# Kernel optimization log

Hardware: AMD Instinct MI355X
Metric: run time of the kernel (lower is better)

Reference implementation:

```python
import jax, jax.numpy as jnp
import numpy as np

SEQ, D, H = 4096, 1024, 1024


def setup_inputs() -> dict:
    key = jax.random.key(0)
    k_x, k_w1, k_b1, k_w2, k_b2 = jax.random.split(key, 5)
    std = 1.0 / np.sqrt(H)
    inputs = jax.random.normal(k_x, (SEQ, D), dtype=jnp.float32)
    W1 = jax.random.uniform(k_w1, (3 * H, 2 * D), minval=-std, maxval=std, dtype=jnp.float32)
    b1 = jax.random.uniform(k_b1, (3 * H,), minval=-std, maxval=std, dtype=jnp.float32)
    W2 = jax.random.uniform(k_w2, (H, H), minval=-std, maxval=std, dtype=jnp.float32)
    b2 = jax.random.uniform(k_b2, (H,), minval=-std, maxval=std, dtype=jnp.float32)
    return {"inputs": inputs, "W1": W1, "b1": b1, "W2": W2, "b2": b2}


def reference(inputs, W1, b1, W2, b2):
    # Exclusive prefix sum along seq: s[t] = sum_{i<t} x[i]
    s = jnp.concatenate(
        [jnp.zeros((1, inputs.shape[1]), dtype=inputs.dtype),
         jnp.cumsum(inputs[:-1], axis=0)], axis=0)
    v = jnp.concatenate([inputs, s], axis=1)            # [S, 2D]
    gates = v @ W1.T + b1                               # [S, 3H]
    ig, fg, h = jnp.split(gates, 3, axis=1)
    ig = jax.nn.sigmoid(ig)
    fg = jax.nn.sigmoid(fg)
    h = jnp.tanh(h) @ W2.T + b2                         # [S, H]
    hr = h * ig
    return (fg, hr)
```

## Files before the change

### kernel.cpp

```cpp
#include <hip/hip_runtime.h>
#include <cmath>

#define S_SEQ 4096
#define HD 1024
#define NG 3072
#define CHR 32
#define NCH 128

typedef _Float16 half8_t __attribute__((ext_vector_type(8)));
typedef _Float16 half4_t __attribute__((ext_vector_type(4)));
typedef float f32x4_t __attribute__((ext_vector_type(4)));

__device__ __forceinline__ void gload_lds16(const void* g, void* l) {
  __builtin_amdgcn_global_load_lds(
      (const __attribute__((address_space(1))) void*)g,
      (__attribute__((address_space(3))) void*)l, 16, 0, 0);
}

__device__ __forceinline__ float sigmoidf_(float x) {
  return 1.f / (1.f + __expf(-x));
}
__device__ __forceinline__ float tanhf_(float x) {
  return 1.f - 2.f / (__expf(2.f * x) + 1.f);
}

#define CONV_BLOCKS 7168
__global__ void prep(const float* __restrict__ W1, const float* __restrict__ W2,
                     _Float16* __restrict__ w1h, _Float16* __restrict__ w2h,
                     const float* __restrict__ x, _Float16* __restrict__ A,
                     _Float16* __restrict__ xsum) {
  const int bid = blockIdx.x;
  if (bid < CONV_BLOCKS) {
    const int n1 = NG * 2048 / 4;
    int i = bid * 256 + threadIdx.x;
    const float* src = (i < n1) ? (W1 + (size_t)i * 4)
                                : (W2 + (size_t)(i - n1) * 4);
    _Float16* dst = (i < n1) ? (w1h + (size_t)i * 4)
                             : (w2h + (size_t)(i - n1) * 4);
    float4 v = *(const float4*)src;
    half4_t h;
    h[0] = (_Float16)v.x; h[1] = (_Float16)v.y;
    h[2] = (_Float16)v.z; h[3] = (_Float16)v.w;
    *(half4_t*)dst = h;
  } else {
    const int sx = bid - CONV_BLOCKS;
    const int j = (sx & 3) * 256 + threadIdx.x;
    const int c = sx >> 2;
    const int t0 = c * CHR;
    float run = 0.f;
    for (int t = t0; t < t0 + CHR; ++t) {
      float v = x[(size_t)t * HD + j];
      A[(size_t)t * 2048 + j]        = (_Float16)v;
      A[(size_t)t * 2048 + 1024 + j] = (_Float16)run;
      run += v;
    }
    xsum[(size_t)c * HD + j] = (_Float16)run;
  }
}

__global__ void scan_part(const float* __restrict__ praw,
                          const float* __restrict__ b1,
                          float* __restrict__ pout) {
  int j = blockIdx.x * 256 + threadIdx.x;
  const size_t SP = (size_t)NCH * NG;
  float run = b1[j];
  for (int c = 0; c < NCH; c += 8) {
    float v[8];
#pragma unroll
    for (int u = 0; u < 8; ++u) {
      size_t i0 = (size_t)(c + u) * NG + j;
      v[u] = (praw[i0] + praw[i0 + SP]) + (praw[i0 + 2 * SP] + praw[i0 + 3 * SP]);
    }
#pragma unroll
    for (int u = 0; u < 8; ++u) {
      pout[(size_t)(c + u) * NG + j] = run;
      run += v[u];
    }
  }
}

__global__ __launch_bounds__(256, 2)
void gemm_part(const _Float16* __restrict__ A, const _Float16* __restrict__ B,
               float* __restrict__ C) {
  __shared__ _Float16 As[128 * 32];
  __shared__ _Float16 Bs[128 * 32];

  const int tid = threadIdx.x;
  const int lane = tid & 63;
  const int wid = tid >> 6;
  const int wr = wid >> 1;
  const int wc = wid & 1;

  const int n0 = blockIdx.x * 128;
  const int koff = blockIdx.z * 256;

  const int srow = lane >> 2;
  const int scol = (lane & 3) << 3;

  const _Float16* gA = A + (size_t)(wid * 32 + srow) * 1024 + koff + scol;
  const _Float16* gB = B + (size_t)(n0 + wid * 32 + srow) * 2048 + koff + scol;
  _Float16* lA = As + (wid * 32) * 32;
  _Float16* lB = Bs + (wid * 32) * 32;

  f32x4_t acc[4][4] = {};

  const int fr = lane & 15;
  const int fk = (lane >> 4) << 3;

  for (int kk = 0; kk < 256; kk += 32) {
    gload_lds16(gA + kk,                    lA);
    gload_lds16(gA + kk + (size_t)16*1024,  lA + 16 * 32);
    gload_lds16(gB + kk,                    lB);
    gload_lds16(gB + kk + (size_t)16*2048,  lB + 16 * 32);
    __syncthreads();

    half8_t af[4], bf[4];
#pragma unroll
    for (int m = 0; m < 4; ++m)
      af[m] = *(const half8_t*)&As[(wr * 64 + m * 16 + fr) * 32 + fk];
#pragma unroll
    for (int n = 0; n < 4; ++n)
      bf[n] = *(const half8_t*)&Bs[(wc * 64 + n * 16 + fr) * 32 + fk];
#pragma unroll
    for (int m = 0; m < 4; ++m)
#pragma unroll
      for (int n = 0; n < 4; ++n)
        acc[m][n] = __builtin_amdgcn_mfma_f32_16x16x32_f16(af[m], bf[n],
                                                           acc[m][n], 0, 0, 0);
    __syncthreads();
  }

  float* Cz = C + (size_t)blockIdx.z * NCH * NG;
  const int crow = wr * 64 + ((lane >> 4) << 2);
  const int ccol = n0 + wc * 64 + fr;
#pragma unroll
  for (int m = 0; m < 4; ++m)
#pragma unroll
    for (int n = 0; n < 4; ++n) {
      const int col = ccol + n * 16;
#pragma unroll
      for (int r = 0; r < 4; ++r)
        Cz[(size_t)(crow + m * 16 + r) * NG + col] = acc[m][n][r];
    }
}

#define BARX __builtin_amdgcn_s_barrier()
#define PR1 __builtin_amdgcn_s_setprio(1)
#define PR0 __builtin_amdgcn_s_setprio(0)
#define VM4 asm volatile("s_waitcnt vmcnt(4)" ::: "memory")

template <int NTILE, int MODE>
__global__ __launch_bounds__(256, 3)
void gemm_t3(const _Float16* __restrict__ A, const _Float16* __restrict__ B,
             int N,
             const float* __restrict__ part, _Float16* __restrict__ igb,
             float* __restrict__ outf, _Float16* __restrict__ th,
             const float* __restrict__ bias, const _Float16* __restrict__ mulh) {
  constexpr int KS = NTILE * 32;
  __shared__ __align__(16) _Float16 sA[3][128 * 32];
  __shared__ __align__(16) _Float16 sB[3][128 * 32];

  const int tid = threadIdx.x;
  const int l = tid & 63;
  const int wid = tid >> 6;
  const int wr = wid >> 1;
  const int wc = wid & 1;
  const int m0 = blockIdx.y * 128;
  const int n0 = blockIdx.x * 128;

  const int srow = tid >> 2;
  const int schunk = (tid & 3) ^ ((tid >> 3) & 3);
  const _Float16* gA = A + (size_t)(m0 + srow) * KS + schunk * 8;
  const _Float16* gB = B + (size_t)(n0 + srow) * KS + schunk * 8;
  const int ldst = tid * 8;

#define STG(bn, kt) do {                                              \
    const int kk_ = (kt) * 32;                                        \
    gload_lds16(gA + kk_,           &sA[bn][ldst]);                   \
    gload_lds16(gA + kk_ + 64 * KS, &sA[bn][2048 + ldst]);            \
    gload_lds16(gB + kk_,           &sB[bn][ldst]);                   \
    gload_lds16(gB + kk_ + 64 * KS, &sB[bn][2048 + ldst]);            \
  } while (0)

  const int fr = l & 15;
  const int kidx = (((l >> 4) ^ ((l >> 1) & 3)) << 3);

  f32x4_t acc[4][4] = {};

#define BODY(kt, bc, bn) do {                                         \
    int ks_ = (kt) + 2; if (ks_ > NTILE - 1) ks_ = NTILE - 1;         \
    STG(bn, ks_);                                                     \
    half8_t af[4], bf[4];                                             \
    _Pragma("unroll")                                                 \
    for (int m = 0; m < 4; ++m)                                       \
      af[m] = *(const half8_t*)&sA[bc][(wr*64 + m*16 + fr)*32 + kidx];\
    _Pragma("unroll")                                                 \
    for (int n = 0; n < 4; ++n)                                       \
      bf[n] = *(const half8_t*)&sB[bc][(wc*64 + n*16 + fr)*32 + kidx];\
    PR1;                                                              \
    _Pragma("unroll")                                                 \
    for (int m = 0; m < 4; ++m)                                       \
      _Pragma("unroll")                                               \
      for (int n = 0; n < 4; ++n)                                     \
        acc[m][n] = __builtin_amdgcn_mfma_f32_16x16x32_f16(           \
            af[m], bf[n], acc[m][n], 0, 0, 0);                        \
    PR0;                                                              \
    VM4; BARX;                                                        \
  } while (0)

  STG(0, 0);
  STG(1, 1);
  VM4; BARX;

#pragma unroll 1
  for (int t3 = 0; t3 < NTILE / 3; ++t3) {
    const int kt = t3 * 3;
    BODY(kt,     0, 2);
    BODY(kt + 1, 1, 0);
    BODY(kt + 2, 2, 1);
  }
  if constexpr (NTILE % 3 >= 1) BODY(NTILE - NTILE % 3,     0, 2);
  if constexpr (NTILE % 3 >= 2) BODY(NTILE - NTILE % 3 + 1, 1, 0);

  const int crow = m0 + wr * 64 + ((l >> 4) << 2);
  const int ccol = n0 + wc * 64 + fr;
#pragma unroll
  for (int m = 0; m < 4; ++m)
#pragma unroll
    for (int n = 0; n < 4; ++n) {
      const int col = ccol + n * 16;
#pragma unroll
      for (int r = 0; r < 4; ++r) {
        const int row = crow + m * 16 + r;
        const float v = acc[m][n][r];
        if (MODE == 1) {
          size_t idx = (size_t)row * N + col;
          outf[idx] = (v + bias[col]) * (float)mulh[idx];
        } else {
          float g = v + part[(size_t)(row >> 5) * NG + col];
          if (col < 1024)
            igb[(size_t)row * HD + col] = (_Float16)sigmoidf_(g);
          else if (col < 2048)
            outf[(size_t)row * HD + (col - 1024)] = sigmoidf_(g);
          else
            th[(size_t)row * HD + (col - 2048)] = (_Float16)tanhf_(g);
        }
      }
    }
#undef STG
#undef BODY
}

extern "C" void kernel_launch(void* const* d_in, const int* in_sizes, int n_in,
                              void* d_out, int out_size, void* d_ws, size_t ws_size,
                              hipStream_t stream) {
  const float* x  = (const float*)d_in[0];
  const float* W1 = (const float*)d_in[1];
  const float* b1 = (const float*)d_in[2];
  const float* W2 = (const float*)d_in[3];
  const float* b2 = (const float*)d_in[4];
  float* out0 = (float*)d_out;
  float* out1 = out0 + (size_t)S_SEQ * HD;

  char* ws = (char*)d_ws;
  _Float16* Ah    = (_Float16*)(ws);
  _Float16* w1h   = (_Float16*)(ws + ((size_t)16 << 20));
  _Float16* w2h   = (_Float16*)(ws + ((size_t)28 << 20));
  _Float16* xsumh = (_Float16*)(ws + ((size_t)30 << 20));
  float*    praw4 = (float*)   (ws + ((size_t)31 << 20));
  float*    pout  = (float*)   (ws + ((size_t)37 << 20));
  _Float16* igb   = (_Float16*)(ws + ((size_t)39 << 20));
  _Float16* th    = (_Float16*)(ws + ((size_t)47 << 20));

  prep<<<dim3(CONV_BLOCKS + 512), dim3(256), 0, stream>>>(
      W1, W2, w1h, w2h, x, Ah, xsumh);

  gemm_part<<<dim3(NG / 128, 1, 4), dim3(256), 0, stream>>>(
      xsumh, w1h + 1024, praw4);

  scan_part<<<dim3(NG / 256), dim3(256), 0, stream>>>(praw4, b1, pout);

  gemm_t3<64, 2><<<dim3(NG / 128, S_SEQ / 128), dim3(256), 0, stream>>>(
      Ah, w1h, NG, pout, igb, out0, th, nullptr, nullptr);

  gemm_t3<32, 1><<<dim3(HD / 128, S_SEQ / 128), dim3(256), 0, stream>>>(
      th, w2h, HD, nullptr, nullptr, out1, nullptr, b2, igb);
}
```

Baseline: 147.7 us.

## Replace first GEMM with 256x256-tile 8-wave phased kernel; vectorize prefix prep

The main gates GEMM moves from a 128x128 tile, triple-buffered kernel to a 512-thread kernel that computes a 256x256 tile with K=64 stages. It double-buffers in LDS, interleaves the global-to-LDS loads with four MFMA quarter-phases separated by barriers, and remaps block IDs so neighbouring blocks share tiles for cache reuse. The chunked prefix-sum prep is also vectorized to float4 per thread, using fewer blocks. The larger tile is meant to raise arithmetic intensity and cut redundant loads, at the cost of one wave of 192 blocks and heavier register and LDS use.

```diff
diff --git a/kernel.cpp b/kernel.cpp
--- a/kernel.cpp
+++ b/kernel.cpp
@@ -6,6 +6,7 @@
 #define NG 3072
 #define CHR 32
 #define NCH 128
+#define NT1 32
 
 typedef _Float16 half8_t __attribute__((ext_vector_type(8)));
 typedef _Float16 half4_t __attribute__((ext_vector_type(4)));
@@ -43,18 +44,25 @@
     h[2] = (_Float16)v.z; h[3] = (_Float16)v.w;
     *(half4_t*)dst = h;
   } else {
-    const int sx = bid - CONV_BLOCKS;
-    const int j = (sx & 3) * 256 + threadIdx.x;
-    const int c = sx >> 2;
+    const int c = bid - CONV_BLOCKS;
+    const int j = threadIdx.x * 4;
     const int t0 = c * CHR;
-    float run = 0.f;
+    float4 run = make_float4(0.f, 0.f, 0.f, 0.f);
     for (int t = t0; t < t0 + CHR; ++t) {
-      float v = x[(size_t)t * HD + j];
-      A[(size_t)t * 2048 + j]        = (_Float16)v;
-      A[(size_t)t * 2048 + 1024 + j] = (_Float16)run;
-      run += v;
-    }
-    xsum[(size_t)c * HD + j] = (_Float16)run;
+      float4 v = *(const float4*)&x[(size_t)t * HD + j];
+      half4_t hx, hs;
+      hx[0] = (_Float16)v.x;   hx[1] = (_Float16)v.y;
+      hx[2] = (_Float16)v.z;   hx[3] = (_Float16)v.w;
+      hs[0] = (_Float16)run.x; hs[1] = (_Float16)run.y;
+      hs[2] = (_Float16)run.z; hs[3] = (_Float16)run.w;
+      *(half4_t*)&A[(size_t)t * 2048 + j] = hx;
+      *(half4_t*)&A[(size_t)t * 2048 + 1024 + j] = hs;
+      run.x += v.x; run.y += v.y; run.z += v.z; run.w += v.w;
+    }
+    half4_t hxs;
+    hxs[0] = (_Float16)run.x; hxs[1] = (_Float16)run.y;
+    hxs[2] = (_Float16)run.z; hxs[3] = (_Float16)run.w;
+    *(half4_t*)&xsum[(size_t)c * HD + j] = hxs;
   }
 }
 
@@ -148,14 +156,15 @@
 #define PR1 __builtin_amdgcn_s_setprio(1)
 #define PR0 __builtin_amdgcn_s_setprio(0)
 #define VM4 asm volatile("s_waitcnt vmcnt(4)" ::: "memory")
-
-template <int NTILE, int MODE>
+#define VM6 asm volatile("s_waitcnt vmcnt(6)" ::: "memory")
+#define LGKM0 asm volatile("s_waitcnt lgkmcnt(0)" ::: "memory")
+#define SB0 __builtin_amdgcn_sched_barrier(0)
+
+template <int NTILE>
 __global__ __launch_bounds__(256, 3)
-void gemm_t3(const _Float16* __restrict__ A, const _Float16* __restrict__ B,
-             int N,
-             const float* __restrict__ part, _Float16* __restrict__ igb,
-             float* __restrict__ outf, _Float16* __restrict__ th,
-             const float* __restrict__ bias, const _Float16* __restrict__ mulh) {
+void gemm2_t3(const _Float16* __restrict__ A, const _Float16* __restrict__ B,
+              int N, float* __restrict__ outf,
+              const float* __restrict__ bias, const _Float16* __restrict__ mulh) {
   constexpr int KS = NTILE * 32;
   __shared__ __align__(16) _Float16 sA[3][128 * 32];
   __shared__ __align__(16) _Float16 sB[3][128 * 32];
@@ -232,23 +241,159 @@
 #pragma unroll
       for (int r = 0; r < 4; ++r) {
         const int row = crow + m * 16 + r;
-        const float v = acc[m][n][r];
-        if (MODE == 1) {
-          size_t idx = (size_t)row * N + col;
-          outf[idx] = (v + bias[col]) * (float)mulh[idx];
-        } else {
-          float g = v + part[(size_t)(row >> 5) * NG + col];
-          if (col < 1024)
-            igb[(size_t)row * HD + col] = (_Float16)sigmoidf_(g);
-          else if (col < 2048)
-            outf[(size_t)row * HD + (col - 1024)] = sigmoidf_(g);
-          else
-            th[(size_t)row * HD + (col - 2048)] = (_Float16)tanhf_(g);
-        }
+        size_t idx = (size_t)row * N + col;
+        outf[idx] = (acc[m][n][r] + bias[col]) * (float)mulh[idx];
       }
     }
 #undef STG
 #undef BODY
+}
+
+__global__ __launch_bounds__(512)
+void gemm1_8ph(const _Float16* __restrict__ A, const _Float16* __restrict__ B,
+               const float* __restrict__ part, _Float16* __restrict__ igb,
+               float* __restrict__ out0, _Float16* __restrict__ th) {
+  __shared__ __align__(16) _Float16 sA[2][256 * 64];
+  __shared__ __align__(16) _Float16 sB[2][256 * 64];
+
+  const int tid = threadIdx.x;
+  const int l = tid & 63;
+  const int w = tid >> 6;
+  const int wr = w >> 2;
+  const int wc = w & 3;
+
+  const int id = blockIdx.x;
+  const int swz = (id & 7) * 24 + (id >> 3);
+  const int bx = swz % 12;
+  const int by = swz / 12;
+  const int m0 = by * 256;
+  const int n0 = bx * 256;
+
+  const int lr = l >> 3;
+  const int lcs = ((l & 7) ^ lr) << 3;
+  const _Float16* gA0 =
+      A + (size_t)(m0 + (w >> 2) * 128 + (w & 3) * 16 + lr) * 2048 + lcs;
+  const _Float16* gB0 =
+      B + (size_t)(n0 + (w >> 1) * 64 + (w & 1) * 16 + lr) * 2048 + lcs;
+  const int dsoA = ((w >> 2) * 128 + (w & 3) * 16) * 64;
+  const int dsoB = ((w >> 1) * 64 + (w & 1) * 16) * 64;
+
+#define STG_A(bb, h, tt) do {                                          \
+    const _Float16* gs_ = gA0 + (size_t)(h) * 64 * 2048 + (tt) * 64;   \
+    _Float16* ds_ = &sA[bb][dsoA + (h) * 4096];                        \
+    gload_lds16(gs_, ds_);                                             \
+    gload_lds16(gs_ + 8 * 2048, ds_ + 512);                            \
+  } while (0)
+#define STG_B(bb, h, tt) do {                                          \
+    const _Float16* gs_ = gB0 + (size_t)(h) * 32 * 2048 + (tt) * 64;   \
+    _Float16* ds_ = &sB[bb][dsoB + (h) * 2048];                        \
+    gload_lds16(gs_, ds_);                                             \
+    gload_lds16(gs_ + 8 * 2048, ds_ + 512);                            \
+  } while (0)
+
+  const int sw = (l & 7) << 3;
+  const int k0 = (l >> 4) << 3;
+
+#define RDA(dst, mb, kh, bb)                                                  \
+    dst = *(const half8_t*)&sA[bb][(((wr * 128 + (mb) * 16 + (l & 15)) * 64)  \
+                                    + k0 + (kh) * 32) ^ sw];
+#define RDB(dst, nb, kh, bb)                                                  \
+    dst = *(const half8_t*)&sB[bb][(((wc * 64 + (nb) * 16 + (l & 15)) * 64)   \
+                                    + k0 + (kh) * 32) ^ sw];
+
+  f32x4_t acc[2][2][4][2] = {};
+
+#define MMQ(MH, NH, AF, BF) do {                                      \
+    _Pragma("unroll")                                                 \
+    for (int m = 0; m < 4; ++m)                                       \
+      _Pragma("unroll")                                               \
+      for (int n = 0; n < 2; ++n) {                                   \
+        acc[MH][NH][m][n] = __builtin_amdgcn_mfma_f32_16x16x32_f16(   \
+            AF[m][0], BF[n][0], acc[MH][NH][m][n], 0, 0, 0);          \
+        acc[MH][NH][m][n] = __builtin_amdgcn_mfma_f32_16x16x32_f16(   \
+            AF[m][1], BF[n][1], acc[MH][NH][m][n], 0, 0, 0);          \
+      }                                                               \
+  } while (0)
+
+  half8_t alo[4][2], ahi[4][2], blo[2][2], bhi[2][2];
+
+  STG_A(0, 0, 0); STG_B(0, 0, 0); STG_B(0, 1, 0); STG_A(0, 1, 0);
+  STG_A(1, 0, 1); STG_B(1, 0, 1); STG_B(1, 1, 1);
+  VM6; BARX;
+
+#define TILE(T, BUF) do {                                             \
+    const int t1_ = ((T) + 1 < NT1) ? (T) + 1 : NT1 - 1;              \
+    const int t2_ = ((T) + 2 < NT1) ? (T) + 2 : NT1 - 1;              \
+                \
+    _Pragma("unroll")                                                 \
+    for (int m = 0; m < 4; ++m) {                                     \
+      RDA(alo[m][0], m, 0, BUF); RDA(alo[m][1], m, 1, BUF);           \
+    }                                                                 \
+    _Pragma("unroll")                                                 \
+    for (int n = 0; n < 2; ++n) {                                     \
+      RDB(blo[n][0], n, 0, BUF); RDB(blo[n][1], n, 1, BUF);           \
+    }                                                                 \
+    STG_A((BUF) ^ 1, 1, t1_);                                         \
+    SB0; BARX; LGKM0; SB0;                                            \
+    PR1; MMQ(0, 0, alo, blo); PR0; BARX;                              \
+          \
+    _Pragma("unroll")                                                 \
+    for (int n = 0; n < 2; ++n) {                                     \
+      RDB(bhi[n][0], 2 + n, 0, BUF); RDB(bhi[n][1], 2 + n, 1, BUF);   \
+    }                                                                 \
+    STG_A(BUF, 0, t2_);                                               \
+    SB0; BARX; LGKM0; SB0;                                            \
+    PR1; MMQ(0, 1, alo, bhi); PR0; BARX;                              \
+                        \
+    _Pragma("unroll")                                                 \
+    for (int m = 0; m < 4; ++m) {                                     \
+      RDA(ahi[m][0], 4 + m, 0, BUF); RDA(ahi[m][1], 4 + m, 1, BUF);   \
+    }                                                                 \
+    STG_B(BUF, 0, t2_);                                               \
+    SB0; BARX; LGKM0; SB0;                                            \
+    PR1; MMQ(1, 0, ahi, blo); PR0; BARX;                              \
+                   \
+    STG_B(BUF, 1, t2_);                                               \
+    BARX;                                                             \
+    PR1; MMQ(1, 1, ahi, bhi); PR0; VM6; BARX;                         \
+  } while (0)
+
+#pragma unroll 1
+  for (int t = 0; t < NT1; t += 2) {
+    TILE(t, 0);
+    TILE(t + 1, 1);
+  }
+
+  const int region = n0 >> 10;
+  const int cb = n0 & 1023;
+#pragma unroll
+  for (int mh = 0; mh < 2; ++mh)
+#pragma unroll
+    for (int m = 0; m < 4; ++m) {
+      const int rbase = m0 + wr * 128 + mh * 64 + m * 16 + ((l >> 4) << 2);
+#pragma unroll
+      for (int r = 0; r < 4; ++r) {
+        const int grow = rbase + r;
+        const float* prow = part + (size_t)(grow >> 5) * NG + n0;
+#pragma unroll
+        for (int nh = 0; nh < 2; ++nh)
+#pragma unroll
+          for (int n = 0; n < 2; ++n) {
+            const int lc = wc * 64 + nh * 32 + n * 16 + (l & 15);
+            const float g = acc[mh][nh][m][n][r] + prow[lc];
+            const size_t oi = (size_t)grow * HD + cb + lc;
+            if (region == 0)      igb[oi] = (_Float16)sigmoidf_(g);
+            else if (region == 1) out0[oi] = sigmoidf_(g);
+            else                  th[oi] = (_Float16)tanhf_(g);
+          }
+      }
+    }
+#undef STG_A
+#undef STG_B
+#undef RDA
+#undef RDB
+#undef MMQ
+#undef TILE
 }
 
 extern "C" void kernel_launch(void* const* d_in, const int* in_sizes, int n_in,
@@ -272,7 +417,7 @@
   _Float16* igb   = (_Float16*)(ws + ((size_t)39 << 20));
   _Float16* th    = (_Float16*)(ws + ((size_t)47 << 20));
 
-  prep<<<dim3(CONV_BLOCKS + 512), dim3(256), 0, stream>>>(
+  prep<<<dim3(CONV_BLOCKS + 128), dim3(256), 0, stream>>>(
       W1, W2, w1h, w2h, x, Ah, xsumh);
 
   gemm_part<<<dim3(NG / 128, 1, 4), dim3(256), 0, stream>>>(
@@ -280,9 +425,9 @@
 
   scan_part<<<dim3(NG / 256), dim3(256), 0, stream>>>(praw4, b1, pout);
 
-  gemm_t3<64, 2><<<dim3(NG / 128, S_SEQ / 128), dim3(256), 0, stream>>>(
-      Ah, w1h, NG, pout, igb, out0, th, nullptr, nullptr);
-
-  gemm_t3<32, 1><<<dim3(HD / 128, S_SEQ / 128), dim3(256), 0, stream>>>(
-      th, w2h, HD, nullptr, nullptr, out1, nullptr, b2, igb);
-}
+  gemm1_8ph<<<dim3(192), dim3(512), 0, stream>>>(
+      Ah, w1h, pout, igb, out0, th);
+
+  gemm2_t3<32><<<dim3(HD / 128, S_SEQ / 128), dim3(256), 0, stream>>>(
+      th, w2h, HD, out1, b2, igb);
+}
```

After: 156.3 us. 1.06x slower.

## Swizzle gate GEMM blocks per XCD, split chunk GEMM K eightfold, vectorize prep

Applied to the files above, without the earlier changes.

The gate GEMM now uses a 1D grid remapped so each XCD handles a contiguous band of row tiles, which should improve L2 reuse of A tiles. The chunk-sum GEMM splits K into 8 slices instead of 4 for more parallelism, and the scan sums 8 partials. The prep scan now uses float4 per thread over 128 blocks, and the epilogue preloads the prefix-bias values into registers once. Costs are extra partial-buffer traffic and a reliance on a fixed round-robin XCD assignment.

```diff
diff --git a/kernel.cpp b/kernel.cpp
--- a/kernel.cpp
+++ b/kernel.cpp
@@ -6,6 +6,7 @@
 #define NG 3072
 #define CHR 32
 #define NCH 128
+#define NZ 8
 
 typedef _Float16 half8_t __attribute__((ext_vector_type(8)));
 typedef _Float16 half4_t __attribute__((ext_vector_type(4)));
@@ -43,18 +44,25 @@
     h[2] = (_Float16)v.z; h[3] = (_Float16)v.w;
     *(half4_t*)dst = h;
   } else {
-    const int sx = bid - CONV_BLOCKS;
-    const int j = (sx & 3) * 256 + threadIdx.x;
-    const int c = sx >> 2;
+    const int c = bid - CONV_BLOCKS;
+    const int j = threadIdx.x * 4;
     const int t0 = c * CHR;
-    float run = 0.f;
+    float4 run = make_float4(0.f, 0.f, 0.f, 0.f);
     for (int t = t0; t < t0 + CHR; ++t) {
-      float v = x[(size_t)t * HD + j];
-      A[(size_t)t * 2048 + j]        = (_Float16)v;
-      A[(size_t)t * 2048 + 1024 + j] = (_Float16)run;
-      run += v;
-    }
-    xsum[(size_t)c * HD + j] = (_Float16)run;
+      float4 v = *(const float4*)&x[(size_t)t * HD + j];
+      half4_t hx, hs;
+      hx[0] = (_Float16)v.x;   hx[1] = (_Float16)v.y;
+      hx[2] = (_Float16)v.z;   hx[3] = (_Float16)v.w;
+      hs[0] = (_Float16)run.x; hs[1] = (_Float16)run.y;
+      hs[2] = (_Float16)run.z; hs[3] = (_Float16)run.w;
+      *(half4_t*)&A[(size_t)t * 2048 + j] = hx;
+      *(half4_t*)&A[(size_t)t * 2048 + 1024 + j] = hs;
+      run.x += v.x; run.y += v.y; run.z += v.z; run.w += v.w;
+    }
+    half4_t hxs;
+    hxs[0] = (_Float16)run.x; hxs[1] = (_Float16)run.y;
+    hxs[2] = (_Float16)run.z; hxs[3] = (_Float16)run.w;
+    *(half4_t*)&xsum[(size_t)c * HD + j] = hxs;
   }
 }
 
@@ -69,7 +77,11 @@
 #pragma unroll
     for (int u = 0; u < 8; ++u) {
       size_t i0 = (size_t)(c + u) * NG + j;
-      v[u] = (praw[i0] + praw[i0 + SP]) + (praw[i0 + 2 * SP] + praw[i0 + 3 * SP]);
+      float s0 = praw[i0] + praw[i0 + SP];
+      float s1 = praw[i0 + 2 * SP] + praw[i0 + 3 * SP];
+      float s2 = praw[i0 + 4 * SP] + praw[i0 + 5 * SP];
+      float s3 = praw[i0 + 6 * SP] + praw[i0 + 7 * SP];
+      v[u] = (s0 + s1) + (s2 + s3);
     }
 #pragma unroll
     for (int u = 0; u < 8; ++u) {
@@ -92,7 +104,7 @@
   const int wc = wid & 1;
 
   const int n0 = blockIdx.x * 128;
-  const int koff = blockIdx.z * 256;
+  const int koff = blockIdx.z * (1024 / NZ);
 
   const int srow = lane >> 2;
   const int scol = (lane & 3) << 3;
@@ -107,7 +119,7 @@
   const int fr = lane & 15;
   const int fk = (lane >> 4) << 3;
 
-  for (int kk = 0; kk < 256; kk += 32) {
+  for (int kk = 0; kk < 1024 / NZ; kk += 32) {
     gload_lds16(gA + kk,                    lA);
     gload_lds16(gA + kk + (size_t)16*1024,  lA + 16 * 32);
     gload_lds16(gB + kk,                    lB);
@@ -149,7 +161,7 @@
 #define PR0 __builtin_amdgcn_s_setprio(0)
 #define VM4 asm volatile("s_waitcnt vmcnt(4)" ::: "memory")
 
-template <int NTILE, int MODE>
+template <int NTILE, int MODE, int SWZ, int NBX>
 __global__ __launch_bounds__(256, 3)
 void gemm_t3(const _Float16* __restrict__ A, const _Float16* __restrict__ B,
              int N,
@@ -165,8 +177,20 @@
   const int wid = tid >> 6;
   const int wr = wid >> 1;
   const int wc = wid & 1;
-  const int m0 = blockIdx.y * 128;
-  const int n0 = blockIdx.x * 128;
+
+  int bx, by;
+  if constexpr (SWZ) {
+    const int bid = blockIdx.x;
+    const int xcd = bid & 7;
+    const int q = bid >> 3;
+    by = xcd * 4 + q / NBX;
+    bx = q % NBX;
+  } else {
+    bx = blockIdx.x;
+    by = blockIdx.y;
+  }
+  const int m0 = by * 128;
+  const int n0 = bx * 128;
 
   const int srow = tid >> 2;
   const int schunk = (tid & 3) ^ ((tid >> 3) & 3);
@@ -224,6 +248,17 @@
 
   const int crow = m0 + wr * 64 + ((l >> 4) << 2);
   const int ccol = n0 + wc * 64 + fr;
+
+  float pv[2][4];
+  if constexpr (MODE == 2) {
+    const int cbase = crow >> 5;
+#pragma unroll
+    for (int h = 0; h < 2; ++h)
+#pragma unroll
+      for (int n = 0; n < 4; ++n)
+        pv[h][n] = part[(size_t)(cbase + h) * NG + ccol + n * 16];
+  }
+
 #pragma unroll
   for (int m = 0; m < 4; ++m)
 #pragma unroll
@@ -237,7 +272,7 @@
           size_t idx = (size_t)row * N + col;
           outf[idx] = (v + bias[col]) * (float)mulh[idx];
         } else {
-          float g = v + part[(size_t)(row >> 5) * NG + col];
+          float g = v + pv[m >> 1][n];
           if (col < 1024)
             igb[(size_t)row * HD + col] = (_Float16)sigmoidf_(g);
           else if (col < 2048)
@@ -267,22 +302,22 @@
   _Float16* w1h   = (_Float16*)(ws + ((size_t)16 << 20));
   _Float16* w2h   = (_Float16*)(ws + ((size_t)28 << 20));
   _Float16* xsumh = (_Float16*)(ws + ((size_t)30 << 20));
-  float*    praw4 = (float*)   (ws + ((size_t)31 << 20));
-  float*    pout  = (float*)   (ws + ((size_t)37 << 20));
-  _Float16* igb   = (_Float16*)(ws + ((size_t)39 << 20));
-  _Float16* th    = (_Float16*)(ws + ((size_t)47 << 20));
-
-  prep<<<dim3(CONV_BLOCKS + 512), dim3(256), 0, stream>>>(
+  float*    praw  = (float*)   (ws + ((size_t)31 << 20));
+  float*    pout  = (float*)   (ws + ((size_t)43 << 20));
+  _Float16* igb   = (_Float16*)(ws + ((size_t)45 << 20));
+  _Float16* th    = (_Float16*)(ws + ((size_t)53 << 20));
+
+  prep<<<dim3(CONV_BLOCKS + 128), dim3(256), 0, stream>>>(
       W1, W2, w1h, w2h, x, Ah, xsumh);
 
-  gemm_part<<<dim3(NG / 128, 1, 4), dim3(256), 0, stream>>>(
-      xsumh, w1h + 1024, praw4);
-
-  scan_part<<<dim3(NG / 256), dim3(256), 0, stream>>>(praw4, b1, pout);
-
-  gemm_t3<64, 2><<<dim3(NG / 128, S_SEQ / 128), dim3(256), 0, stream>>>(
+  gemm_part<<<dim3(NG / 128, 1, NZ), dim3(256), 0, stream>>>(
+      xsumh, w1h + 1024, praw);
+
+  scan_part<<<dim3(NG / 256), dim3(256), 0, stream>>>(praw, b1, pout);
+
+  gemm_t3<64, 2, 1, NG / 128><<<dim3(768), dim3(256), 0, stream>>>(
       Ah, w1h, NG, pout, igb, out0, th, nullptr, nullptr);
 
-  gemm_t3<32, 1><<<dim3(HD / 128, S_SEQ / 128), dim3(256), 0, stream>>>(
+  gemm_t3<32, 1, 0, 0><<<dim3(HD / 128, S_SEQ / 128), dim3(256), 0, stream>>>(
       th, w2h, HD, nullptr, nullptr, out1, nullptr, b2, igb);
 }
```

Result: no change. 149.1 us (+1.0%).
